# Kernel tuning notes

Measured on AMD Instinct MI355X. Metric: run time of the kernel, lower is better.

Reference implementation:

```python
import jax, jax.numpy as jnp
import numpy as np


def setup_inputs() -> dict:
    key = jax.random.key(0)
    ks = jax.random.split(key, 4)
    B, C, H, W = 8, 256, 64, 64
    Cq = C // 8
    x = jax.random.normal(ks[0], (B, C, H, W), dtype=jnp.float32)
    wq = jax.random.normal(ks[1], (Cq, C), dtype=jnp.float32) * (1.0 / np.sqrt(C))
    bq = jnp.zeros((Cq,), dtype=jnp.float32)
    wk = jax.random.normal(ks[2], (Cq, C), dtype=jnp.float32) * (1.0 / np.sqrt(C))
    bk = jnp.zeros((Cq,), dtype=jnp.float32)
    wv = jax.random.normal(ks[3], (C, C), dtype=jnp.float32) * (1.0 / np.sqrt(C))
    bv = jnp.zeros((C,), dtype=jnp.float32)
    return {"x": x, "wq": wq, "bq": bq, "wk": wk, "bk": bk, "wv": wv, "bv": bv}


def reference(x, wq, bq, wk, bk, wv, bv):
    B, C, H, W = x.shape
    N = H * W
    xf = x.reshape(B, C, N)  # [B, C, N] ; 1x1 conv == channel matmul
    q = jnp.einsum('bcn,dc->bnd', xf, wq) + bq          # [B, N, Cq]
    k = jnp.einsum('bcn,dc->bdn', xf, wk) + bk[:, None]  # [B, Cq, N]
    v = jnp.einsum('bcn,dc->bdn', xf, wv) + bv[:, None]  # [B, C, N]
    energy = jnp.einsum('bnd,bdm->bnm', q, k)           # [B, N, N]
    attn = jax.nn.softmax(energy, axis=-1)              # softmax over keys
    # out[b,c,i] = sum_j v[b,c,j] * attn[b,i,j]
    out = jnp.einsum('bcj,bij->bci', v, attn).reshape(B, C, H, W)
    return x + out
```

## Files before the change

kernel.cpp:

```cpp
#include <hip/hip_runtime.h>


#define CH  256
#define DQ  32
#define NSP 4096
#define RWS 320

typedef short short8 __attribute__((ext_vector_type(8)));
typedef float float4v __attribute__((ext_vector_type(4)));

__device__ __forceinline__ unsigned short f2b(float f) {
  unsigned int u = __float_as_uint(f);
  unsigned int r = u + 0x7fffu + ((u >> 16) & 1u);
  return (unsigned short)(r >> 16);
}
__device__ __forceinline__ short8 ld8(const unsigned short* p) {
  return *(const short8*)p;
}

__global__ __launch_bounds__(256) void prep_kernel(
    const float* __restrict__ wq, const float* __restrict__ bq,
    const float* __restrict__ wk, const float* __restrict__ bk,
    const float* __restrict__ wv, const float* __restrict__ bv,
    unsigned short* __restrict__ wh, unsigned short* __restrict__ wl,
    float* __restrict__ ball) {
  int r = blockIdx.x, c = threadIdx.x;
  float v;
  if (r < 32)       v = wq[r * CH + c];
  else if (r < 64)  v = wk[(r - 32) * CH + c];
  else              v = wv[(r - 64) * CH + c];
  unsigned int u = __float_as_uint(v);
  unsigned short hi = (unsigned short)(u >> 16);
  float hf = __uint_as_float(u & 0xffff0000u);
  unsigned short lo = (unsigned short)(__float_as_uint(v - hf) >> 16);
  wh[r * CH + c] = hi;
  wl[r * CH + c] = lo;
  if (c == 0)
    ball[r] = (r < 32) ? bq[r] : (r < 64 ? bk[r - 32] : bv[r - 64]);
}

__device__ __forceinline__ void stage_x(const float* xkn, float* buf,
                                        int w, int lane) {
#pragma unroll
  for (int i = 0; i < 2; ++i) {
    const int h  = 2 * w + i;
    const int sw = ((h >> 1) & 1) * 16;
    const int c  = h * 4 + (lane >> 4);
    const int n  = ((lane & 15) * 4) ^ sw;
    const float* gp = xkn + (size_t)c * NSP + n;
    __builtin_amdgcn_global_load_lds(
        (const __attribute__((address_space(1))) unsigned int*)gp,
        (__attribute__((address_space(3))) unsigned int*)(buf + h * 256),
        16, 0, 0);
  }
}

__global__ __launch_bounds__(256, 2) void proj_kernel(
    const float* __restrict__ x,
    const unsigned short* __restrict__ wh, const unsigned short* __restrict__ wl,
    const float* __restrict__ ball,
    unsigned short* __restrict__ qb, unsigned short* __restrict__ kb,
    unsigned short* __restrict__ vb, int b0) {
  __shared__ float xs[8][2048];

  const int bz   = blockIdx.z;
  const int bg   = b0 + bz;
  const int n0   = blockIdx.x * 64;
  const int t    = threadIdx.x;
  const int w    = t >> 6;
  const int lane = t & 63;
  const int col  = lane & 15;
  const int quad = lane >> 4;
  const int r0   = 80 * w;
  const int e    = (quad & 1) * 16;
  const int lbase = quad * 512 + col;

  const float* xb = x + (size_t)bg * CH * NSP;

#pragma unroll
  for (int ks = 0; ks < 8; ++ks)
    stage_x(xb + (size_t)(ks * 32) * NSP + n0, xs[ks], w, lane);

  float4v acc[5][4];
#pragma unroll
  for (int rf = 0; rf < 5; ++rf) {
    float bias = ball[r0 + 16 * rf + col];
#pragma unroll
    for (int ns = 0; ns < 4; ++ns)
      acc[rf][ns] = (float4v){bias, bias, bias, bias};
  }

  __syncthreads();

#pragma unroll
  for (int ks = 0; ks < 8; ++ks) {
    const int k0 = ks * 32;

    short8 wfh[5], wfl[5];
#pragma unroll
    for (int rf = 0; rf < 5; ++rf) {
      size_t wo = (size_t)(r0 + 16 * rf + col) * CH + k0 + quad * 8;
      wfh[rf] = ld8(wh + wo);
      wfl[rf] = ld8(wl + wo);
    }

    const float* xc = &xs[ks][0];
    short8 ah[4], al[4];
#pragma unroll
    for (int nsb = 0; nsb < 4; ++nsb) {
      const float* xp2 = xc + lbase + ((nsb * 16) ^ e);
#pragma unroll
      for (int j = 0; j < 8; ++j) {
        float v = xp2[j * 64];
        unsigned int u = __float_as_uint(v);
        ah[nsb][j] = (short)(u >> 16);
        float hf = __uint_as_float(u & 0xffff0000u);
        al[nsb][j] = (short)(__float_as_uint(v - hf) >> 16);
      }
    }

#pragma unroll
    for (int rf = 0; rf < 5; ++rf)
#pragma unroll
      for (int ns = 0; ns < 4; ++ns) {
        acc[rf][ns] = __builtin_amdgcn_mfma_f32_16x16x32_bf16(ah[ns], wfh[rf], acc[rf][ns], 0, 0, 0);
        acc[rf][ns] = __builtin_amdgcn_mfma_f32_16x16x32_bf16(al[ns], wfh[rf], acc[rf][ns], 0, 0, 0);
        acc[rf][ns] = __builtin_amdgcn_mfma_f32_16x16x32_bf16(ah[ns], wfl[rf], acc[rf][ns], 0, 0, 0);
      }
  }

  __syncthreads();

#pragma unroll
  for (int rf = 0; rf < 5; ++rf) {
    const int rr = r0 + 16 * rf + col;
    const int rb = r0 + 16 * rf;
    if (rb >= 64) {
#pragma unroll
      for (int ns = 0; ns < 4; ++ns) {
        const int nb = n0 + ns * 16 + quad * 4;
        ushort4 o = {f2b(acc[rf][ns][0]), f2b(acc[rf][ns][1]),
                     f2b(acc[rf][ns][2]), f2b(acc[rf][ns][3])};
        *(ushort4*)&vb[((size_t)bz * CH + (rr - 64)) * NSP + nb] = o;
      }
    }
  }

  if (w == 0) {
    unsigned short* qt = (unsigned short*)&xs[0][0];
#pragma unroll
    for (int rf = 0; rf < 4; ++rf) {
      const int rr = 16 * rf + col;
#pragma unroll
      for (int ns = 0; ns < 4; ++ns) {
#pragma unroll
        for (int reg = 0; reg < 4; ++reg)
          qt[(16 * ns + quad * 4 + reg) * 68 + rr] = f2b(acc[rf][ns][reg]);
      }
    }
    const int nl = lane >> 3;
    const int c4 = (lane & 7) * 4;
#pragma unroll
    for (int it = 0; it < 8; ++it) {
      const int n = 8 * it + nl;
      ushort4 vq = *(const ushort4*)&qt[n * 68 + c4];
      ushort4 vk = *(const ushort4*)&qt[n * 68 + 32 + c4];
      *(ushort4*)&qb[((size_t)bz * NSP + n0 + n) * DQ + c4] = vq;
      *(ushort4*)&kb[((size_t)bz * NSP + n0 + n) * DQ + c4] = vk;
    }
  }
}

__global__ __launch_bounds__(512, 4) void attn_kernel(
    const float* __restrict__ x,
    const unsigned short* __restrict__ qb, const unsigned short* __restrict__ kb,
    const unsigned short* __restrict__ vb,
    float* __restrict__ out, int b0, int ns) {
  __shared__ unsigned short ps[2 * 64 * 64];
  __shared__ float buf[4][64];
  __shared__ float lf[64];

  const int bl   = blockIdx.x % ns;
  const int bg   = b0 + bl;
  const int i0   = (blockIdx.x / ns) * 64;
  const int t    = threadIdx.x;
  const int w    = t >> 6;
  const int rh   = w >> 2;
  const int kq   = w & 3;
  const int lane = t & 63;
  const int col  = lane & 15;
  const int quad = lane >> 4;
  const float LOG2E = 1.4426950408889634f;
  const float MOFF  = 57.70780163555852f;

  const unsigned short* qbb = qb + (size_t)bl * NSP * DQ;
  const unsigned short* kbb = kb + (size_t)bl * NSP * DQ;
  const unsigned short* vbb = vb + (size_t)bl * CH * NSP;

  short8 qf[2];
#pragma unroll
  for (int rgp = 0; rgp < 2; ++rgp)
    qf[rgp] = ld8(qbb + (size_t)(i0 + 32 * rh + 16 * rgp + col) * DQ + quad * 8);
  const float4v z4 = (float4v){0.f, 0.f, 0.f, 0.f};

  const int kb8 = 2 * kq + (col >> 3);
  const int ci  = col & 7;
  const int q4  = 4 * (quad & 1);
  const int ob  = quad ^ ci;

  float4v acc[4][2];
#pragma unroll
  for (int rg = 0; rg < 4; ++rg)
#pragma unroll
    for (int ct = 0; ct < 2; ++ct) acc[rg][ct] = z4;
  float lp[2][4];
#pragma unroll
  for (int rgp = 0; rgp < 2; ++rgp)
#pragma unroll
    for (int reg = 0; reg < 4; ++reg) lp[rgp][reg] = 0.0f;

  short8 kf = ld8(kbb + (size_t)(16 * kq + col) * DQ + quad * 8);
  for (int j0 = 0; j0 < NSP; j0 += 64) {
    const int cp = (j0 >> 6) & 1;
    short8 vf[2][2];
#pragma unroll
    for (int ct = 0; ct < 2; ++ct)
#pragma unroll
      for (int h = 0; h < 2; ++h)
        vf[ct][h] = ld8(vbb + (size_t)(32 * w + 16 * ct + col) * NSP
                        + j0 + 32 * h + quad * 8);
    float4v c0 = __builtin_amdgcn_mfma_f32_16x16x32_bf16(qf[0], kf, z4, 0, 0, 0);
    float4v c1 = __builtin_amdgcn_mfma_f32_16x16x32_bf16(qf[1], kf, z4, 0, 0, 0);
    int jn = (j0 + 64 < NSP) ? j0 + 64 : 0;
    short8 kfn = ld8(kbb + (size_t)(jn + 16 * kq + col) * DQ + quad * 8);
    unsigned short* pw = &ps[cp * 4096 + (32 * rh + quad * 4) * 64 + ci];
#pragma unroll
    for (int reg = 0; reg < 4; ++reg) {
      float p0 = __builtin_amdgcn_exp2f(fmaf(c0[reg], LOG2E, -MOFF));
      float p1 = __builtin_amdgcn_exp2f(fmaf(c1[reg], LOG2E, -MOFF));
      lp[0][reg] += p0;
      lp[1][reg] += p1;
      const int so = reg * 64 + (kb8 ^ (q4 + reg)) * 8;
      pw[so]        = f2b(p0);
      pw[so + 1024] = f2b(p1);
    }
    asm volatile("s_waitcnt lgkmcnt(0)" ::: "memory");
    __builtin_amdgcn_s_barrier();
    __builtin_amdgcn_sched_barrier(0);

    const short8* pb0 = (const short8*)&ps[cp * 4096 + col * 64 + ob * 8];
    const short8* pb1 = (const short8*)&ps[cp * 4096 + col * 64 + (ob ^ 4) * 8];
    __builtin_amdgcn_s_setprio(1);
#pragma unroll
    for (int rg = 0; rg < 4; ++rg) {
      short8 pf0 = pb0[rg * 128];
      short8 pf1 = pb1[rg * 128];
#pragma unroll
      for (int ct = 0; ct < 2; ++ct) {
        acc[rg][ct] = __builtin_amdgcn_mfma_f32_16x16x32_bf16(pf0, vf[ct][0], acc[rg][ct], 0, 0, 0);
        acc[rg][ct] = __builtin_amdgcn_mfma_f32_16x16x32_bf16(pf1, vf[ct][1], acc[rg][ct], 0, 0, 0);
      }
    }
    __builtin_amdgcn_s_setprio(0);
    kf = kfn;
  }

#pragma unroll
  for (int rgp = 0; rgp < 2; ++rgp)
#pragma unroll
    for (int reg = 0; reg < 4; ++reg) {
#pragma unroll
      for (int mask = 1; mask <= 8; mask <<= 1)
        lp[rgp][reg] += __shfl_xor(lp[rgp][reg], mask);
    }
  if (col == 0) {
#pragma unroll
    for (int rgp = 0; rgp < 2; ++rgp)
#pragma unroll
      for (int reg = 0; reg < 4; ++reg)
        buf[kq][32 * rh + 16 * rgp + quad * 4 + reg] = lp[rgp][reg];
  }
  __syncthreads();
  if (kq == 0 && col == 0) {
#pragma unroll
    for (int rgp = 0; rgp < 2; ++rgp)
#pragma unroll
      for (int reg = 0; reg < 4; ++reg) {
        int row = 32 * rh + 16 * rgp + quad * 4 + reg;
        lf[row] = 1.0f / (buf[0][row] + buf[1][row] + buf[2][row] + buf[3][row]);
      }
  }
  __syncthreads();

#pragma unroll
  for (int rg = 0; rg < 4; ++rg) {
    float linv[4];
#pragma unroll
    for (int reg = 0; reg < 4; ++reg)
      linv[reg] = lf[16 * rg + quad * 4 + reg];
#pragma unroll
    for (int ct = 0; ct < 2; ++ct) {
      int c  = 32 * w + 16 * ct + col;
      int ib = i0 + 16 * rg + quad * 4;
      size_t idx = ((size_t)bg * CH + c) * NSP + ib;
      float4 xr = *(const float4*)&x[idx];
      float4 o;
      o.x = acc[rg][ct][0] * linv[0] + xr.x;
      o.y = acc[rg][ct][1] * linv[1] + xr.y;
      o.z = acc[rg][ct][2] * linv[2] + xr.z;
      o.w = acc[rg][ct][3] * linv[3] + xr.w;
      *(float4*)&out[idx] = o;
    }
  }
}

extern "C" void kernel_launch(void* const* d_in, const int* in_sizes, int n_in,
                              void* d_out, int out_size, void* d_ws, size_t ws_size,
                              hipStream_t stream) {
  (void)in_sizes; (void)n_in; (void)out_size;
  const float* x  = (const float*)d_in[0];
  const float* wq = (const float*)d_in[1];
  const float* bq = (const float*)d_in[2];
  const float* wk = (const float*)d_in[3];
  const float* bk = (const float*)d_in[4];
  const float* wv = (const float*)d_in[5];
  const float* bv = (const float*)d_in[6];
  float* out = (float*)d_out;

  const size_t WALL_B = (size_t)RWS * CH * sizeof(float) + 4096;
  const size_t QB_B = (size_t)NSP * DQ * sizeof(unsigned short);
  const size_t VB_B = (size_t)CH * NSP * sizeof(unsigned short);
  const size_t PER_B = 2 * QB_B + VB_B;

  int ns = 8;
  while (ns > 1 && WALL_B + (size_t)ns * PER_B > ws_size) ns >>= 1;

  char* ws = (char*)d_ws;
  unsigned short* wh = (unsigned short*)ws;
  unsigned short* wl = wh + (size_t)RWS * CH;
  float* ball = (float*)(ws + (size_t)RWS * CH * 2 * sizeof(unsigned short));
  char* qkv = ws + WALL_B;
  unsigned short* qb = (unsigned short*)qkv;
  unsigned short* kb = (unsigned short*)(qkv + (size_t)ns * QB_B);
  unsigned short* vb = (unsigned short*)(qkv + (size_t)ns * 2 * QB_B);

  prep_kernel<<<dim3(RWS), dim3(256), 0, stream>>>(wq, bq, wk, bk, wv, bv, wh, wl, ball);
  for (int b0 = 0; b0 < 8; b0 += ns) {
    proj_kernel<<<dim3(64, 1, ns), dim3(256), 0, stream>>>(
        x, wh, wl, ball, qb, kb, vb, b0);
    attn_kernel<<<dim3(64 * ns), dim3(512), 0, stream>>>(
        x, qb, kb, vb, out, b0, ns);
  }
}
```

Before: 254.0 us.

## Split attention key range in two and merge partials in a finalize kernel

```diff
diff --git a/kernel.cpp b/kernel.cpp
--- a/kernel.cpp
+++ b/kernel.cpp
@@ -8,6 +8,7 @@
 
 typedef short short8 __attribute__((ext_vector_type(8)));
 typedef float float4v __attribute__((ext_vector_type(4)));
+typedef _Float16 half4v __attribute__((ext_vector_type(4)));
 
 __device__ __forceinline__ unsigned short f2b(float f) {
   unsigned int u = __float_as_uint(f);
@@ -95,7 +96,6 @@
 #pragma unroll
   for (int ks = 0; ks < 8; ++ks) {
     const int k0 = ks * 32;
-
     short8 wfh[5], wfl[5];
 #pragma unroll
     for (int rf = 0; rf < 5; ++rf) {
@@ -103,7 +103,6 @@
       wfh[rf] = ld8(wh + wo);
       wfl[rf] = ld8(wl + wo);
     }
-
     const float* xc = &xs[ks][0];
     short8 ah[4], al[4];
 #pragma unroll
@@ -118,7 +117,6 @@
         al[nsb][j] = (short)(__float_as_uint(v - hf) >> 16);
       }
     }
-
 #pragma unroll
     for (int rf = 0; rf < 5; ++rf)
 #pragma unroll
@@ -175,14 +173,20 @@
     const float* __restrict__ x,
     const unsigned short* __restrict__ qb, const unsigned short* __restrict__ kb,
     const unsigned short* __restrict__ vb,
-    float* __restrict__ out, int b0, int ns) {
+    float* __restrict__ out, _Float16* __restrict__ po,
+    float* __restrict__ pl, int b0, int ns, int ksplit) {
   __shared__ unsigned short ps[2 * 64 * 64];
   __shared__ float buf[4][64];
   __shared__ float lf[64];
 
-  const int bl   = blockIdx.x % ns;
+  const int b    = blockIdx.x;
+  const int bl   = b % ns;
   const int bg   = b0 + bl;
-  const int i0   = (blockIdx.x / ns) * 64;
+  const int kh   = (b / ns) % ksplit;
+  const int i0   = (b / (ns * ksplit)) * 64;
+  const int jlen = NSP / ksplit;
+  const int js   = kh * jlen;
+  const int je   = js + jlen;
   const int t    = threadIdx.x;
   const int w    = t >> 6;
   const int rh   = w >> 2;
@@ -219,8 +223,8 @@
 #pragma unroll
     for (int reg = 0; reg < 4; ++reg) lp[rgp][reg] = 0.0f;
 
-  short8 kf = ld8(kbb + (size_t)(16 * kq + col) * DQ + quad * 8);
-  for (int j0 = 0; j0 < NSP; j0 += 64) {
+  short8 kf = ld8(kbb + (size_t)(js + 16 * kq + col) * DQ + quad * 8);
+  for (int j0 = js; j0 < je; j0 += 64) {
     const int cp = (j0 >> 6) & 1;
     short8 vf[2][2];
 #pragma unroll
@@ -231,7 +235,7 @@
                         + j0 + 32 * h + quad * 8);
     float4v c0 = __builtin_amdgcn_mfma_f32_16x16x32_bf16(qf[0], kf, z4, 0, 0, 0);
     float4v c1 = __builtin_amdgcn_mfma_f32_16x16x32_bf16(qf[1], kf, z4, 0, 0, 0);
-    int jn = (j0 + 64 < NSP) ? j0 + 64 : 0;
+    int jn = (j0 + 64 < je) ? j0 + 64 : js;
     short8 kfn = ld8(kbb + (size_t)(jn + 16 * kq + col) * DQ + quad * 8);
     unsigned short* pw = &ps[cp * 4096 + (32 * rh + quad * 4) * 64 + ci];
 #pragma unroll
@@ -287,30 +291,89 @@
 #pragma unroll
       for (int reg = 0; reg < 4; ++reg) {
         int row = 32 * rh + 16 * rgp + quad * 4 + reg;
-        lf[row] = 1.0f / (buf[0][row] + buf[1][row] + buf[2][row] + buf[3][row]);
+        float ls = buf[0][row] + buf[1][row] + buf[2][row] + buf[3][row];
+        lf[row] = 1.0f / ls;
+        if (ksplit == 2)
+          pl[(size_t)(bl * 2 + kh) * NSP + i0 + row] = ls;
       }
   }
   __syncthreads();
 
-#pragma unroll
-  for (int rg = 0; rg < 4; ++rg) {
-    float linv[4];
-#pragma unroll
-    for (int reg = 0; reg < 4; ++reg)
-      linv[reg] = lf[16 * rg + quad * 4 + reg];
-#pragma unroll
-    for (int ct = 0; ct < 2; ++ct) {
-      int c  = 32 * w + 16 * ct + col;
-      int ib = i0 + 16 * rg + quad * 4;
-      size_t idx = ((size_t)bg * CH + c) * NSP + ib;
-      float4 xr = *(const float4*)&x[idx];
-      float4 o;
-      o.x = acc[rg][ct][0] * linv[0] + xr.x;
-      o.y = acc[rg][ct][1] * linv[1] + xr.y;
-      o.z = acc[rg][ct][2] * linv[2] + xr.z;
-      o.w = acc[rg][ct][3] * linv[3] + xr.w;
-      *(float4*)&out[idx] = o;
-    }
+  if (ksplit == 2) {
+    _Float16* pob = po + (size_t)(bl * 2 + kh) * CH * NSP;
+#pragma unroll
+    for (int rg = 0; rg < 4; ++rg) {
+      float linv[4];
+#pragma unroll
+      for (int reg = 0; reg < 4; ++reg)
+        linv[reg] = lf[16 * rg + quad * 4 + reg];
+#pragma unroll
+      for (int ct = 0; ct < 2; ++ct) {
+        int c  = 32 * w + 16 * ct + col;
+        int ib = i0 + 16 * rg + quad * 4;
+        half4v h;
+        h[0] = (_Float16)(acc[rg][ct][0] * linv[0]);
+        h[1] = (_Float16)(acc[rg][ct][1] * linv[1]);
+        h[2] = (_Float16)(acc[rg][ct][2] * linv[2]);
+        h[3] = (_Float16)(acc[rg][ct][3] * linv[3]);
+        *(half4v*)&pob[(size_t)c * NSP + ib] = h;
+      }
+    }
+  } else {
+#pragma unroll
+    for (int rg = 0; rg < 4; ++rg) {
+      float linv[4];
+#pragma unroll
+      for (int reg = 0; reg < 4; ++reg)
+        linv[reg] = lf[16 * rg + quad * 4 + reg];
+#pragma unroll
+      for (int ct = 0; ct < 2; ++ct) {
+        int c  = 32 * w + 16 * ct + col;
+        int ib = i0 + 16 * rg + quad * 4;
+        size_t idx = ((size_t)bg * CH + c) * NSP + ib;
+        float4 xr = *(const float4*)&x[idx];
+        float4 o;
+        o.x = acc[rg][ct][0] * linv[0] + xr.x;
+        o.y = acc[rg][ct][1] * linv[1] + xr.y;
+        o.z = acc[rg][ct][2] * linv[2] + xr.z;
+        o.w = acc[rg][ct][3] * linv[3] + xr.w;
+        *(float4*)&out[idx] = o;
+      }
+    }
+  }
+}
+
+__global__ __launch_bounds__(256) void fin_kernel(
+    const float* __restrict__ x, const _Float16* __restrict__ po,
+    const float* __restrict__ pl, float* __restrict__ out, int b0, int ns) {
+  const int bl = blockIdx.z;
+  const int bg = b0 + bl;
+  const int i  = blockIdx.x * 256 + (threadIdx.x & 63) * 4;
+  const int c0 = blockIdx.y * 64 + (threadIdx.x >> 6);
+
+  float4 l0 = *(const float4*)&pl[(size_t)(bl * 2) * NSP + i];
+  float4 l1 = *(const float4*)&pl[(size_t)(bl * 2 + 1) * NSP + i];
+  float4 w0, w1;
+  w0.x = l0.x / (l0.x + l1.x);  w1.x = 1.0f - w0.x;
+  w0.y = l0.y / (l0.y + l1.y);  w1.y = 1.0f - w0.y;
+  w0.z = l0.z / (l0.z + l1.z);  w1.z = 1.0f - w0.z;
+  w0.w = l0.w / (l0.w + l1.w);  w1.w = 1.0f - w0.w;
+
+  const size_t khs = (size_t)CH * NSP;
+#pragma unroll
+  for (int cc = 0; cc < 16; ++cc) {
+    const int c = c0 + cc * 4;
+    size_t pidx = ((size_t)(bl * 2) * CH + c) * NSP + i;
+    half4v h0 = *(const half4v*)&po[pidx];
+    half4v h1 = *(const half4v*)&po[pidx + khs];
+    size_t idx = ((size_t)bg * CH + c) * NSP + i;
+    float4 xr = *(const float4*)&x[idx];
+    float4 o;
+    o.x = xr.x + (float)h0[0] * w0.x + (float)h1[0] * w1.x;
+    o.y = xr.y + (float)h0[1] * w0.y + (float)h1[1] * w1.y;
+    o.z = xr.z + (float)h0[2] * w0.z + (float)h1[2] * w1.z;
+    o.w = xr.w + (float)h0[3] * w0.w + (float)h1[3] * w1.w;
+    *(float4*)&out[idx] = o;
   }
 }
 
@@ -330,10 +393,15 @@
   const size_t WALL_B = (size_t)RWS * CH * sizeof(float) + 4096;
   const size_t QB_B = (size_t)NSP * DQ * sizeof(unsigned short);
   const size_t VB_B = (size_t)CH * NSP * sizeof(unsigned short);
+  const size_t PO_B = (size_t)2 * CH * NSP * sizeof(_Float16);
+  const size_t PL_B = (size_t)2 * NSP * sizeof(float);
   const size_t PER_B = 2 * QB_B + VB_B;
 
+  int ksplit = (WALL_B + 8 * (PER_B + PO_B + PL_B) <= ws_size) ? 2 : 1;
+  const size_t PER_T = PER_B + (ksplit == 2 ? PO_B + PL_B : 0);
+
   int ns = 8;
-  while (ns > 1 && WALL_B + (size_t)ns * PER_B > ws_size) ns >>= 1;
+  while (ns > 1 && WALL_B + (size_t)ns * PER_T > ws_size) ns >>= 1;
 
   char* ws = (char*)d_ws;
   unsigned short* wh = (unsigned short*)ws;
@@ -343,12 +411,17 @@
   unsigned short* qb = (unsigned short*)qkv;
   unsigned short* kb = (unsigned short*)(qkv + (size_t)ns * QB_B);
   unsigned short* vb = (unsigned short*)(qkv + (size_t)ns * 2 * QB_B);
+  _Float16* po = (_Float16*)(qkv + (size_t)ns * PER_B);
+  float* pl = (float*)(qkv + (size_t)ns * (PER_B + PO_B));
 
   prep_kernel<<<dim3(RWS), dim3(256), 0, stream>>>(wq, bq, wk, bk, wv, bv, wh, wl, ball);
   for (int b0 = 0; b0 < 8; b0 += ns) {
     proj_kernel<<<dim3(64, 1, ns), dim3(256), 0, stream>>>(
         x, wh, wl, ball, qb, kb, vb, b0);
-    attn_kernel<<<dim3(64 * ns), dim3(512), 0, stream>>>(
-        x, qb, kb, vb, out, b0, ns);
-  }
-}
+    attn_kernel<<<dim3(64 * ksplit * ns), dim3(512), 0, stream>>>(
+        x, qb, kb, vb, out, po, pl, b0, ns, ksplit);
+    if (ksplit == 2)
+      fin_kernel<<<dim3(16, 4, ns), dim3(256), 0, stream>>>(
+          x, po, pl, out, b0, ns);
+  }
+}
```

Result: slower. 269.0 us (+5.9%).
